# Kernel optimization log

Hardware: AMD Instinct MI355X
Metric: run time of the kernel (lower is better)

The kernel has to match this reference:

```python
import jax, jax.numpy as jnp
from jax import lax
import numpy as np

N = 10000      # nodes
T = 60         # lookback window
F = 16         # features per timestep
HL = 256       # lstm hidden dim
GH = 8         # gat heads
GC = 64        # gat out channels per head
GD = GH * GC   # 512 concat dim
FH = 512       # fusion hidden
E = 320000     # edges (before self loops)


def _lstm_layer(x, w_ih, w_hh, b_ih, b_hh):
    # x: [T, N, in] -> hidden sequence [T, N, HL]; torch gate order i,f,g,o
    n = x.shape[1]
    h0 = jnp.zeros((n, HL), x.dtype)
    def step(carry, xt):
        h, c = carry
        g = xt @ w_ih.T + h @ w_hh.T + b_ih + b_hh
        i, f, gg, o = jnp.split(g, 4, axis=-1)
        c = jax.nn.sigmoid(f) * c + jax.nn.sigmoid(i) * jnp.tanh(gg)
        h = jax.nn.sigmoid(o) * jnp.tanh(c)
        return (h, c), h
    _, hs = lax.scan(step, (h0, h0), x)
    return hs


def _gatv2(x, src, dst, ea, wl, bl, wr, br, we, att, bias):
    # GATv2Conv (concat=True, edge_dim=1, negative_slope=0.2); self loops already in src/dst/ea
    n = x.shape[0]
    xl = (x @ wl + bl).reshape(n, GH, GC)   # lin_l (source / x_j)
    xr = (x @ wr + br).reshape(n, GH, GC)   # lin_r (target / x_i)
    ee = (ea @ we).reshape(-1, GH, GC)      # lin_edge (bias=False)
    m = jax.nn.leaky_relu(xl[src] + xr[dst] + ee, 0.2)      # [E', GH, GC]
    logits = jnp.einsum('ehc,hc->eh', m, att)               # [E', GH]
    mx = jax.ops.segment_max(logits, dst, num_segments=n)
    ex = jnp.exp(logits - mx[dst])
    den = jax.ops.segment_sum(ex, dst, num_segments=n)
    alpha = ex / den[dst]                                   # softmax over in-edges per node
    out = jax.ops.segment_sum(xl[src] * alpha[..., None], dst, num_segments=n)
    return out.reshape(n, GD) + bias


def setup_inputs():
    key = jax.random.key(0)
    ks = jax.random.split(key, 20)
    f32 = jnp.float32
    def nrm(k, shp, fan):
        return jax.random.normal(k, shp, f32) * (1.0 / np.sqrt(fan))
    return {
        "x_seq": jax.random.normal(ks[0], (N, T, F), f32),
        "edge_index": jax.random.randint(ks[1], (2, E), 0, N, jnp.int32),
        "edge_attr": jax.random.uniform(ks[2], (E, 1), dtype=f32),
        "w_ih0": nrm(ks[3], (4 * HL, F), HL), "w_hh0": nrm(ks[4], (4 * HL, HL), HL),
        "b_ih0": jnp.zeros((4 * HL,), f32), "b_hh0": jnp.zeros((4 * HL,), f32),
        "w_ih1": nrm(ks[5], (4 * HL, HL), HL), "w_hh1": nrm(ks[6], (4 * HL, HL), HL),
        "b_ih1": jnp.zeros((4 * HL,), f32), "b_hh1": jnp.zeros((4 * HL,), f32),
        "g0_wl": nrm(ks[7], (HL, GD), HL), "g0_bl": jnp.zeros((GD,), f32),
        "g0_wr": nrm(ks[8], (HL, GD), HL), "g0_br": jnp.zeros((GD,), f32),
        "g0_we": nrm(ks[9], (1, GD), 1),
        "g0_att": nrm(ks[10], (GH, GC), GC), "g0_bias": jnp.zeros((GD,), f32),
        "g1_wl": nrm(ks[11], (GD, GD), GD), "g1_bl": jnp.zeros((GD,), f32),
        "g1_wr": nrm(ks[12], (GD, GD), GD), "g1_br": jnp.zeros((GD,), f32),
        "g1_we": nrm(ks[13], (1, GD), 1),
        "g1_att": nrm(ks[14], (GH, GC), GC), "g1_bias": jnp.zeros((GD,), f32),
        "fc1_w": nrm(ks[15], (HL + GD, FH), HL + GD), "fc1_b": jnp.zeros((FH,), f32),
        "fc2_w": nrm(ks[16], (FH, 1), FH), "fc2_b": jnp.zeros((1,), f32),
    }


def reference(x_seq, edge_index, edge_attr,
              w_ih0, w_hh0, b_ih0, b_hh0, w_ih1, w_hh1, b_ih1, b_hh1,
              g0_wl, g0_bl, g0_wr, g0_br, g0_we, g0_att, g0_bias,
              g1_wl, g1_bl, g1_wr, g1_br, g1_we, g1_att, g1_bias,
              fc1_w, fc1_b, fc2_w, fc2_b):
    # 2-layer LSTM encoder, take last timestep hidden (dropout off: eval mode)
    xt = jnp.transpose(x_seq, (1, 0, 2))            # [T, N, F]
    h1 = _lstm_layer(xt, w_ih0, w_hh0, b_ih0, b_hh0)
    h2 = _lstm_layer(h1, w_ih1, w_hh1, b_ih1, b_hh1)
    node = h2[-1]                                    # [N, HL]
    # add self loops; fill edge_attr for loops with mean (PyG default fill_value='mean')
    loop = jnp.arange(N, dtype=edge_index.dtype)
    src = jnp.concatenate([edge_index[0], loop])
    dst = jnp.concatenate([edge_index[1], loop])
    ea = jnp.concatenate([edge_attr, jnp.broadcast_to(edge_attr.mean(axis=0), (N, 1))], axis=0)
    g = jax.nn.elu(_gatv2(node, src, dst, ea, g0_wl, g0_bl, g0_wr, g0_br, g0_we, g0_att, g0_bias))
    g = jax.nn.elu(_gatv2(g, src, dst, ea, g1_wl, g1_bl, g1_wr, g1_br, g1_we, g1_att, g1_bias))
    fused = jnp.concatenate([node, g], axis=1)       # [N, HL+GD]
    h = jax.nn.relu(fused @ fc1_w + fc1_b)
    return h @ fc2_w + fc2_b                         # [N, 1]
```

## Files before the change

kernel.cpp:

```cpp
#include <hip/hip_runtime.h>

#define DEV __device__ __forceinline__

typedef _Float16 f16;
typedef _Float16 f16x8 __attribute__((ext_vector_type(8)));
typedef _Float16 f16x2 __attribute__((ext_vector_type(2)));
typedef float f32x4 __attribute__((ext_vector_type(4)));

DEV float sigmoidf_(float x) { return 1.0f / (1.0f + __expf(-x)); }
DEV float tanhf2_(float x)   { return 1.0f - 2.0f / (__expf(2.0f * x) + 1.0f); }

DEV void load_lds16(const void* g, void* l) {
    __builtin_amdgcn_global_load_lds(
        (const __attribute__((address_space(1))) char*)(const char*)g,
        (__attribute__((address_space(3))) char*)(unsigned int)(unsigned long long)(char*)l,
        16, 0, 0);
}

DEV int swz(int row, int ck) { return ck ^ (row & 3) ^ ((row >> 2) & 3); }

__global__ void prep_w0_kernel(const float* __restrict__ wih,
                               const float* __restrict__ whh,
                               f16* __restrict__ dst) {
    int idx = blockIdx.x * 256 + threadIdx.x;
    if (idx >= 1024 * 320) return;
    int rd = idx / 320, k = idx - rd * 320;
    int T = rd >> 7, p = rd & 127;
    int u = T * 32 + ((p >> 6) & 1) * 16 + (p & 15);
    int g = (p >> 4) & 3;
    int src = g * 256 + u;
    float v;
    if (k < 16)        v = wih[src * 16 + k];
    else if (k < 272)  v = whh[src * 256 + (k - 16)];
    else               v = 0.f;
    dst[idx] = (f16)v;
}

__global__ void prep_w1_kernel(const float* __restrict__ wih,
                               const float* __restrict__ whh,
                               f16* __restrict__ dst) {
    int idx = blockIdx.x * 256 + threadIdx.x;
    if (idx >= 1024 * 512) return;
    int rd = idx >> 9, k = idx & 511;
    int T = rd >> 7, p = rd & 127;
    int u = T * 32 + ((p >> 6) & 1) * 16 + (p & 15);
    int g = (p >> 4) & 3;
    int src = g * 256 + u;
    float v = (k < 256) ? wih[src * 256 + k] : whh[src * 256 + (k - 256)];
    dst[idx] = (f16)v;
}

__global__ void prep_bias4_kernel(const float* __restrict__ bi,
                                  const float* __restrict__ bh,
                                  float* __restrict__ dst) {
    int idx = blockIdx.x * 256 + threadIdx.x;
    if (idx >= 1024) return;
    int u = idx >> 2, g = idx & 3;
    dst[idx] = bi[g * 256 + u] + bh[g * 256 + u];
}

__global__ void prep_wt_kernel(const float* __restrict__ src, f16* __restrict__ dst,
                               int K, int N) {
    int idx = blockIdx.x * 256 + threadIdx.x;
    if (idx >= K * N) return;
    int n = idx / K, k = idx - n * K;
    dst[idx] = (f16)src[(size_t)k * N + n];
}

__global__ void prep_x0_kernel(const float* __restrict__ x_seq, f16* __restrict__ A0,
                               int Nn) {
    int idx = blockIdx.x * 256 + threadIdx.x;
    if (idx >= Nn * 16) return;
    int m = idx >> 4, f = idx & 15;
    A0[(size_t)m * 320 + f] = (f16)x_seq[(size_t)m * 960 + f];
}

DEV void tile_load_chunk(const f16* __restrict__ A, int lda,
                         const f16* __restrict__ Bt, int K,
                         int m0, int n0, int k0,
                         f16* __restrict__ sA, f16* __restrict__ sB,
                         int w, int arow, int achk)
{
#pragma unroll
    for (int c = 0; c < 2; ++c) {
        int R = c * 64 + w * 16;
        load_lds16(A + (size_t)(m0 + R + arow) * lda + k0 + achk, sA + R * 32);
        load_lds16(Bt + (size_t)(n0 + R + arow) * K + k0 + achk, sB + R * 32);
    }
}

DEV void tile_compute_chunk(const f16* __restrict__ sA, const f16* __restrict__ sB,
                            f32x4 (&acc)[4][4], int wr, int wc, int frow, int fsl)
{
    f16x8 af[4], bf[4];
#pragma unroll
    for (int i = 0; i < 4; ++i)
        af[i] = *(const f16x8*)&sA[(wr + i * 16 + frow) * 32 + fsl];
#pragma unroll
    for (int j = 0; j < 4; ++j)
        bf[j] = *(const f16x8*)&sB[(wc + j * 16 + frow) * 32 + fsl];
#pragma unroll
    for (int i = 0; i < 4; ++i)
#pragma unroll
        for (int j = 0; j < 4; ++j)
            acc[i][j] = __builtin_amdgcn_mfma_f32_16x16x32_f16(af[i], bf[j], acc[i][j], 0, 0, 0);
}

DEV void lstm_step_core(
    f16* __restrict__ sA, f16* __restrict__ sB,
    int bx, int by,
    const f16* __restrict__ A, int lda, int K,
    const f16* __restrict__ Wt,
    const float* __restrict__ bias4,
    float* __restrict__ c_state,
    f16* __restrict__ hA, int ldhA, int offhA,
    f16* __restrict__ hB, int ldhB, int offhB,
    const float* __restrict__ xsrc, int tnext,
    int M)
{
    const int tid = threadIdx.x;
    const int w = tid >> 6, lane = tid & 63;
    const int m0 = bx * 128, n0 = by * 128;
    const int arow = lane >> 2;
    const int achk = swz(arow, lane & 3) * 8;
    const int frow = lane & 15, l4 = lane >> 4;
    const int fsl = swz(frow, l4) * 8;
    const int wr = (w >> 1) * 64, wc = (w & 1) * 64;

    const int u = by * 32 + (w & 1) * 16 + (lane & 15);
    const int rbase = m0 + wr + (lane >> 4) * 4;
    float cold[4][4];
#pragma unroll
    for (int i = 0; i < 4; ++i)
#pragma unroll
        for (int r = 0; r < 4; ++r)
            cold[i][r] = c_state[(size_t)(rbase + i * 16 + r) * 256 + u];

    f32x4 acc[4][4] = {};
    const int nch = K >> 5;

    tile_load_chunk(A, lda, Wt, K, m0, n0, 0, sA, sB, w, arow, achk);
    for (int kc = 0; kc < nch; ++kc) {
        __syncthreads();
        const int cur = (kc & 1) * 4096;
        if (kc + 1 < nch) {
            const int nxt = ((kc + 1) & 1) * 4096;
            tile_load_chunk(A, lda, Wt, K, m0, n0, (kc + 1) * 32,
                            sA + nxt, sB + nxt, w, arow, achk);
        }
        tile_compute_chunk(sA + cur, sB + cur, acc, wr, wc, frow, fsl);
    }

    const float4 bb = *(const float4*)&bias4[u * 4];
#pragma unroll
    for (int i = 0; i < 4; ++i) {
#pragma unroll
        for (int r = 0; r < 4; ++r) {
            int m = rbase + i * 16 + r;
            if (m < M) {
                float gi = sigmoidf_(acc[i][0][r] + bb.x);
                float gf = sigmoidf_(acc[i][1][r] + bb.y);
                float gg = tanhf2_(acc[i][2][r] + bb.z);
                float go = sigmoidf_(acc[i][3][r] + bb.w);
                float cn = gf * cold[i][r] + gi * gg;
                c_state[(size_t)m * 256 + u] = cn;
                f16 h = (f16)(go * tanhf2_(cn));
                hA[(size_t)m * ldhA + offhA + u] = h;
                if (hB) hB[(size_t)m * ldhB + offhB + u] = h;
            }
        }
    }
    if (xsrc && by == 0) {
        int row = tid >> 1, fb = (tid & 1) * 8;
        int m = m0 + row;
        if (m < M) {
            const float* xp = xsrc + (size_t)m * 960 + tnext * 16 + fb;
            f16* dp = hB + (size_t)m * ldhB + fb;
#pragma unroll
            for (int q = 0; q < 8; ++q) dp[q] = (f16)xp[q];
        }
    }
}

__global__ __launch_bounds__(256) void lstm_mfma_kernel(
    const f16* __restrict__ A, int lda, int K,
    const f16* __restrict__ Wt, const float* __restrict__ bias4,
    float* __restrict__ c_state,
    f16* __restrict__ hA, int ldhA, int offhA,
    f16* __restrict__ hB, int ldhB, int offhB,
    const float* __restrict__ xsrc, int tnext, int M, int mtiles)
{
    __shared__ __align__(16) f16 sA[2 * 4096];
    __shared__ __align__(16) f16 sB[2 * 4096];
    const int l = blockIdx.x;
    const int xcd = l & 7, q = l >> 3;
    const int y = q & 7, xhi = q >> 3;
    const int x = xhi * 8 + xcd;
    if (x >= mtiles) return;
    lstm_step_core(sA, sB, x, y, A, lda, K, Wt, bias4, c_state,
                   hA, ldhA, offhA, hB, ldhB, offhB, xsrc, tnext, M);
}

__global__ __launch_bounds__(256) void lstm_dual_kernel(
    const f16* __restrict__ A1, const f16* __restrict__ W1t,
    const float* __restrict__ b41, float* __restrict__ c1,
    f16* __restrict__ h1A, int ldh1A, int offh1A,
    const f16* __restrict__ A0, const f16* __restrict__ W0t,
    const float* __restrict__ b40, float* __restrict__ c0,
    f16* __restrict__ h0A, int ldh0A, int offh0A,
    f16* __restrict__ h0B, int ldh0B, int offh0B,
    const float* __restrict__ xsrc, int tnext, int M, int mtiles)
{
    __shared__ __align__(16) f16 sA[2 * 4096];
    __shared__ __align__(16) f16 sB[2 * 4096];
    const int l = blockIdx.x;
    const int xcd = l & 7, q = l >> 3;
    const int yz = q & 15, xhi = q >> 4;
    const int x = xhi * 8 + xcd;
    if (x >= mtiles) return;
    const int y = yz & 7, z = yz >> 3;
    if (z == 0)
        lstm_step_core(sA, sB, x, y, A1, 512, 512, W1t, b41, c1,
                       h1A, ldh1A, offh1A, nullptr, 0, 0, nullptr, 0, M);
    else
        lstm_step_core(sA, sB, x, y, A0, 320, 320, W0t, b40, c0,
                       h0A, ldh0A, offh0A, h0B, ldh0B, offh0B, xsrc, tnext, M);
}

__global__ __launch_bounds__(256) void gemm16_kernel(
    const f16* __restrict__ A, int lda,
    const f16* __restrict__ Bt, int K,
    const float* __restrict__ bias,
    f16* __restrict__ C16, float* __restrict__ C32, int ldc,
    int act, int M)
{
    __shared__ __align__(16) f16 sA[2 * 4096];
    __shared__ __align__(16) f16 sB[2 * 4096];
    const int tid = threadIdx.x;
    const int w = tid >> 6, lane = tid & 63;
    const int m0 = blockIdx.x * 128, n0 = blockIdx.y * 128;
    const int arow = lane >> 2;
    const int achk = swz(arow, lane & 3) * 8;
    const int frow = lane & 15, l4 = lane >> 4;
    const int fsl = swz(frow, l4) * 8;
    const int wr = (w >> 1) * 64, wcn = (w & 1) * 64;

    f32x4 acc[4][4] = {};
    const int nch = K >> 5;

    tile_load_chunk(A, lda, Bt, K, m0, n0, 0, sA, sB, w, arow, achk);
    for (int kc = 0; kc < nch; ++kc) {
        __syncthreads();
        const int cur = (kc & 1) * 4096;
        if (kc + 1 < nch) {
            const int nxt = ((kc + 1) & 1) * 4096;
            tile_load_chunk(A, lda, Bt, K, m0, n0, (kc + 1) * 32,
                            sA + nxt, sB + nxt, w, arow, achk);
        }
        tile_compute_chunk(sA + cur, sB + cur, acc, wr, wcn, frow, fsl);
    }

    const int rbase = m0 + wr + (lane >> 4) * 4;
#pragma unroll
    for (int i = 0; i < 4; ++i) {
#pragma unroll
        for (int r = 0; r < 4; ++r) {
            int m = rbase + i * 16 + r;
            if (m >= M) continue;
#pragma unroll
            for (int j = 0; j < 4; ++j) {
                int n = n0 + wcn + j * 16 + (lane & 15);
                float v = acc[i][j][r] + bias[n];
                if (act == 1) v = fmaxf(v, 0.f);
                if (C16) C16[(size_t)m * ldc + n] = (f16)v;
                else     C32[(size_t)m * ldc + n] = v;
            }
        }
    }
}

__global__ __launch_bounds__(256) void gemm16_dual_kernel(
    const f16* __restrict__ A, int lda,
    const f16* __restrict__ Btl, const f16* __restrict__ Btr, int K,
    const float* __restrict__ biasl, const float* __restrict__ biasr,
    f16* __restrict__ Cl, f16* __restrict__ Cr, int ldc, int M)
{
    __shared__ __align__(16) f16 sA[2 * 4096];
    __shared__ __align__(16) f16 sB[2 * 4096];
    const int side = blockIdx.y >> 2;
    const f16* Bt = side ? Btr : Btl;
    const float* bias = side ? biasr : biasl;
    f16* C16 = side ? Cr : Cl;
    const int tid = threadIdx.x;
    const int w = tid >> 6, lane = tid & 63;
    const int m0 = blockIdx.x * 128, n0 = (blockIdx.y & 3) * 128;
    const int arow = lane >> 2;
    const int achk = swz(arow, lane & 3) * 8;
    const int frow = lane & 15, l4 = lane >> 4;
    const int fsl = swz(frow, l4) * 8;
    const int wr = (w >> 1) * 64, wcn = (w & 1) * 64;

    f32x4 acc[4][4] = {};
    const int nch = K >> 5;

    tile_load_chunk(A, lda, Bt, K, m0, n0, 0, sA, sB, w, arow, achk);
    for (int kc = 0; kc < nch; ++kc) {
        __syncthreads();
        const int cur = (kc & 1) * 4096;
        if (kc + 1 < nch) {
            const int nxt = ((kc + 1) & 1) * 4096;
            tile_load_chunk(A, lda, Bt, K, m0, n0, (kc + 1) * 32,
                            sA + nxt, sB + nxt, w, arow, achk);
        }
        tile_compute_chunk(sA + cur, sB + cur, acc, wr, wcn, frow, fsl);
    }

    const int rbase = m0 + wr + (lane >> 4) * 4;
#pragma unroll
    for (int i = 0; i < 4; ++i) {
#pragma unroll
        for (int r = 0; r < 4; ++r) {
            int m = rbase + i * 16 + r;
            if (m >= M) continue;
#pragma unroll
            for (int j = 0; j < 4; ++j) {
                int n = n0 + wcn + j * 16 + (lane & 15);
                float v = acc[i][j][r] + bias[n];
                C16[(size_t)m * ldc + n] = (f16)v;
            }
        }
    }
}

__global__ void mean_sum_kernel(const float* __restrict__ a, int n, float* __restrict__ out) {
    __shared__ float s[256];
    float loc = 0.f;
    for (int i = blockIdx.x * 256 + threadIdx.x; i < n; i += gridDim.x * 256) loc += a[i];
    s[threadIdx.x] = loc;
    __syncthreads();
    for (int off = 128; off; off >>= 1) {
        if (threadIdx.x < off) s[threadIdx.x] += s[threadIdx.x + off];
        __syncthreads();
    }
    if (threadIdx.x == 0) atomicAdd(out, s[0]);
}

__global__ void hist_kernel(const int* __restrict__ ei, int Ne, int Nn,
                            int* __restrict__ counts) {
    int e = blockIdx.x * 256 + threadIdx.x;
    if (e >= Ne + Nn) return;
    int d = (e < Ne) ? ei[Ne + e] : (e - Ne);
    atomicAdd(&counts[d], 1);
}

__global__ void scan_kernel(const int* __restrict__ counts, int* __restrict__ offsets, int n) {
    __shared__ int s[256];
    int tid = threadIdx.x;
    int chunk = (n + 255) / 256;
    int b = tid * chunk;
    int loc = 0;
    for (int j = 0; j < chunk; ++j) { int i = b + j; if (i < n) loc += counts[i]; }
    s[tid] = loc;
    __syncthreads();
    for (int off = 1; off < 256; off <<= 1) {
        int v = (tid >= off) ? s[tid - off] : 0;
        __syncthreads();
        s[tid] += v;
        __syncthreads();
    }
    int run = (tid == 0) ? 0 : s[tid - 1];
    for (int j = 0; j < chunk; ++j) {
        int i = b + j;
        if (i < n) { offsets[i] = run; run += counts[i]; }
    }
    if (tid == 255) offsets[n] = run;
}

__global__ void scatter_kernel(const int* __restrict__ ei, const float* __restrict__ ea,
                               const float* __restrict__ sump, float inv_ne, int Ne, int Nn,
                               int* __restrict__ cursor, int* __restrict__ src_sorted,
                               float* __restrict__ ea_sorted) {
    int e = blockIdx.x * 256 + threadIdx.x;
    if (e >= Ne + Nn) return;
    int s, d; float a;
    if (e < Ne) { s = ei[e]; d = ei[Ne + e]; a = ea[e]; }
    else        { s = e - Ne; d = s; a = sump[0] * inv_ne; }
    int pos = atomicAdd(&cursor[d], 1);
    src_sorted[pos] = s;
    ea_sorted[pos] = a;
}

__global__ __launch_bounds__(256) void gat_aggregate_kernel(
    const f16* __restrict__ xl, const f16* __restrict__ xr,
    const float* __restrict__ we, const float* __restrict__ att,
    const float* __restrict__ bias,
    const int* __restrict__ offsets, const int* __restrict__ src_sorted,
    const float* __restrict__ ea_sorted,
    float* __restrict__ logit_buf, f16* __restrict__ out, int ldo, int N)
{
    __shared__ float s_xr[512], s_we[512], s_att[512];
    __shared__ float s_wmax[32], s_mx[8], s_den[8], s_rden[8];
    __shared__ float s_alpha[256];
    __shared__ int s_src[32];
    const int i = blockIdx.x;
    const int tid = threadIdx.x;
    s_xr[tid]       = (float)xr[(size_t)i * 512 + tid];
    s_xr[tid + 256] = (float)xr[(size_t)i * 512 + tid + 256];
    s_we[tid] = we[tid]; s_we[tid + 256] = we[tid + 256];
    s_att[tid] = att[tid]; s_att[tid + 256] = att[tid + 256];
    if (tid < 8) s_den[tid] = 0.f;
    __syncthreads();

    const int beg = offsets[i], end = offsets[i + 1];
    const int w = tid >> 6, lane = tid & 63;

    float wm[4] = {-1e30f, -1e30f, -1e30f, -1e30f};
    for (int e = beg + w; e < end; e += 4) {
        int s = src_sorted[e];
        float a = ea_sorted[e];
        float part[4];
#pragma unroll
        for (int cc = 0; cc < 4; ++cc) {
            int col = cc * 128 + lane * 2;
            f16x2 xv = *(const f16x2*)&xl[(size_t)s * 512 + col];
            float v0 = (float)xv.x + s_xr[col]     + a * s_we[col];
            float v1 = (float)xv.y + s_xr[col + 1] + a * s_we[col + 1];
            v0 = (v0 > 0.f) ? v0 : 0.2f * v0;
            v1 = (v1 > 0.f) ? v1 : 0.2f * v1;
            part[cc] = v0 * s_att[col] + v1 * s_att[col + 1];
        }
#pragma unroll
        for (int off = 16; off; off >>= 1)
#pragma unroll
            for (int cc = 0; cc < 4; ++cc) part[cc] += __shfl_xor(part[cc], off);
        if ((lane & 31) == 0) {
            int hb = lane >> 5;
#pragma unroll
            for (int cc = 0; cc < 4; ++cc) {
                logit_buf[(size_t)e * 8 + 2 * cc + hb] = part[cc];
                wm[cc] = fmaxf(wm[cc], part[cc]);
            }
        }
    }
    if ((lane & 31) == 0) {
        int hb = lane >> 5;
#pragma unroll
        for (int cc = 0; cc < 4; ++cc) s_wmax[w * 8 + 2 * cc + hb] = wm[cc];
    }
    __syncthreads();
    if (tid < 8) {
        float m = fmaxf(fmaxf(s_wmax[tid], s_wmax[8 + tid]),
                        fmaxf(s_wmax[16 + tid], s_wmax[24 + tid]));
        s_mx[tid] = m;
    }
    __syncthreads();

    for (int e = beg + tid; e < end; e += 256) {
#pragma unroll
        for (int h = 0; h < 8; ++h) {
            float ex = __expf(logit_buf[(size_t)e * 8 + h] - s_mx[h]);
            logit_buf[(size_t)e * 8 + h] = ex;
            atomicAdd(&s_den[h], ex);
        }
    }
    __syncthreads();
    if (tid < 8) s_rden[tid] = 1.f / s_den[tid];
    __syncthreads();

    float acc0 = 0.f, acc1 = 0.f;
    const int c2 = tid * 2, hh = tid >> 5;
    for (int chunk = beg; chunk < end; chunk += 32) {
        int cnt = min(32, end - chunk);
        if (tid < cnt) s_src[tid] = src_sorted[chunk + tid];
        int eo = tid >> 3, hq = tid & 7;
        if (eo < cnt) s_alpha[tid] = logit_buf[(size_t)(chunk + eo) * 8 + hq] * s_rden[hq];
        __syncthreads();
        for (int j = 0; j < cnt; ++j) {
            int s = s_src[j];
            f16x2 xv = *(const f16x2*)&xl[(size_t)s * 512 + c2];
            float al = s_alpha[j * 8 + hh];
            acc0 += al * (float)xv.x;
            acc1 += al * (float)xv.y;
        }
        __syncthreads();
    }
    float v0 = acc0 + bias[c2];
    float v1 = acc1 + bias[c2 + 1];
    v0 = (v0 > 0.f) ? v0 : __expf(v0) - 1.f;
    v1 = (v1 > 0.f) ? v1 : __expf(v1) - 1.f;
    f16x2 ov; ov.x = (f16)v0; ov.y = (f16)v1;
    *(f16x2*)&out[(size_t)i * ldo + c2] = ov;
}

__global__ void fc2_kernel(const float* __restrict__ H, const float* __restrict__ w,
                           const float* __restrict__ b, float* __restrict__ out, int N) {
    int wv = threadIdx.x >> 6, lane = threadIdx.x & 63;
    int node = blockIdx.x * 4 + wv;
    if (node >= N) return;
    float s = 0.f;
#pragma unroll
    for (int j = 0; j < 8; ++j)
        s += H[(size_t)node * 512 + j * 64 + lane] * w[j * 64 + lane];
#pragma unroll
    for (int off = 32; off; off >>= 1) s += __shfl_xor(s, off, 64);
    if (lane == 0) out[node] = s + b[0];
}

extern "C" void kernel_launch(void* const* d_in, const int* in_sizes, int n_in,
                              void* d_out, int out_size, void* d_ws, size_t ws_size,
                              hipStream_t stream) {
    const float* x_seq     = (const float*)d_in[0];
    const int*   edge_index= (const int*)d_in[1];
    const float* edge_attr = (const float*)d_in[2];
    const float* w_ih0 = (const float*)d_in[3];
    const float* w_hh0 = (const float*)d_in[4];
    const float* b_ih0 = (const float*)d_in[5];
    const float* b_hh0 = (const float*)d_in[6];
    const float* w_ih1 = (const float*)d_in[7];
    const float* w_hh1 = (const float*)d_in[8];
    const float* b_ih1 = (const float*)d_in[9];
    const float* b_hh1 = (const float*)d_in[10];
    const float* g0_wl = (const float*)d_in[11];
    const float* g0_bl = (const float*)d_in[12];
    const float* g0_wr = (const float*)d_in[13];
    const float* g0_br = (const float*)d_in[14];
    const float* g0_we = (const float*)d_in[15];
    const float* g0_att= (const float*)d_in[16];
    const float* g0_bias=(const float*)d_in[17];
    const float* g1_wl = (const float*)d_in[18];
    const float* g1_bl = (const float*)d_in[19];
    const float* g1_wr = (const float*)d_in[20];
    const float* g1_br = (const float*)d_in[21];
    const float* g1_we = (const float*)d_in[22];
    const float* g1_att= (const float*)d_in[23];
    const float* g1_bias=(const float*)d_in[24];
    const float* fc1_w = (const float*)d_in[25];
    const float* fc1_b = (const float*)d_in[26];
    const float* fc2_w = (const float*)d_in[27];
    const float* fc2_b = (const float*)d_in[28];
    float* out = (float*)d_out;

    const int Nn = in_sizes[0] / (60 * 16);
    const int Ne = in_sizes[1] / 2;
    const int Etot = Ne + Nn;
    const int MT = (Nn + 127) / 128;
    const int Mpad = MT * 128;
    const int MTpad8 = ((MT + 7) / 8) * 8;

    size_t off = 0;
    auto alloc = [&](size_t bytes) -> void* {
        void* r = (char*)d_ws + off;
        off += (bytes + 255) & ~(size_t)255;
        return r;
    };
    f16* W0t   = (f16*)alloc((size_t)1024 * 320 * 2);
    f16* W1t   = (f16*)alloc((size_t)1024 * 512 * 2);
    float* b40 = (float*)alloc(1024 * 4);
    float* b41 = (float*)alloc(1024 * 4);
    f16* Wg0l  = (f16*)alloc((size_t)512 * 256 * 2);
    f16* Wg0r  = (f16*)alloc((size_t)512 * 256 * 2);
    f16* Wg1l  = (f16*)alloc((size_t)512 * 512 * 2);
    f16* Wg1r  = (f16*)alloc((size_t)512 * 512 * 2);
    f16* Wfc1  = (f16*)alloc((size_t)512 * 768 * 2);
    f16* A0b[2]; A0b[0] = (f16*)alloc((size_t)Mpad * 320 * 2);
                 A0b[1] = (f16*)alloc((size_t)Mpad * 320 * 2);
    f16* A1b[2]; A1b[0] = (f16*)alloc((size_t)Mpad * 512 * 2);
                 A1b[1] = (f16*)alloc((size_t)Mpad * 512 * 2);
    float* c0  = (float*)alloc((size_t)Mpad * 256 * 4);
    float* c1  = (float*)alloc((size_t)Mpad * 256 * 4);
    f16* fused = (f16*)alloc((size_t)Mpad * 768 * 2);
    f16* xlbuf = (f16*)alloc((size_t)Mpad * 512 * 2);
    f16* xrbuf = (f16*)alloc((size_t)Mpad * 512 * 2);
    f16* gbuf  = (f16*)alloc((size_t)Mpad * 512 * 2);
    float* hfc1= (float*)alloc((size_t)Mpad * 512 * 4);
    float* logit_buf = (float*)alloc((size_t)Etot * 8 * 4);
    int* counts  = (int*)alloc((size_t)Nn * 4);
    int* offsets = (int*)alloc((size_t)(Nn + 1) * 4);
    int* cursor  = (int*)alloc((size_t)Nn * 4);
    int* src_sorted = (int*)alloc((size_t)Etot * 4);
    float* ea_sorted = (float*)alloc((size_t)Etot * 4);
    float* meanp = (float*)alloc(256);

    prep_w0_kernel<<<dim3((1024 * 320 + 255) / 256), 256, 0, stream>>>(w_ih0, w_hh0, W0t);
    prep_w1_kernel<<<dim3((1024 * 512 + 255) / 256), 256, 0, stream>>>(w_ih1, w_hh1, W1t);
    prep_bias4_kernel<<<dim3(4), 256, 0, stream>>>(b_ih0, b_hh0, b40);
    prep_bias4_kernel<<<dim3(4), 256, 0, stream>>>(b_ih1, b_hh1, b41);
    prep_wt_kernel<<<dim3((256 * 512 + 255) / 256), 256, 0, stream>>>(g0_wl, Wg0l, 256, 512);
    prep_wt_kernel<<<dim3((256 * 512 + 255) / 256), 256, 0, stream>>>(g0_wr, Wg0r, 256, 512);
    prep_wt_kernel<<<dim3((512 * 512 + 255) / 256), 256, 0, stream>>>(g1_wl, Wg1l, 512, 512);
    prep_wt_kernel<<<dim3((512 * 512 + 255) / 256), 256, 0, stream>>>(g1_wr, Wg1r, 512, 512);
    prep_wt_kernel<<<dim3((768 * 512 + 255) / 256), 256, 0, stream>>>(fc1_w, Wfc1, 768, 512);
    hipMemsetAsync(A0b[0], 0, (size_t)Mpad * 320 * 2, stream);
    hipMemsetAsync(A0b[1], 0, (size_t)Mpad * 320 * 2, stream);
    hipMemsetAsync(A1b[0], 0, (size_t)Mpad * 512 * 2, stream);
    hipMemsetAsync(c0, 0, (size_t)Mpad * 256 * 4, stream);
    hipMemsetAsync(c1, 0, (size_t)Mpad * 256 * 4, stream);
    prep_x0_kernel<<<dim3((Nn * 16 + 255) / 256), 256, 0, stream>>>(x_seq, A0b[0], Nn);

    hipMemsetAsync(meanp, 0, 4, stream);
    hipMemsetAsync(counts, 0, (size_t)Nn * 4, stream);
    mean_sum_kernel<<<dim3(256), 256, 0, stream>>>(edge_attr, Ne, meanp);
    hist_kernel<<<dim3((Etot + 255) / 256), 256, 0, stream>>>(edge_index, Ne, Nn, counts);
    scan_kernel<<<dim3(1), 256, 0, stream>>>(counts, offsets, Nn);
    hipMemcpyAsync(cursor, offsets, (size_t)Nn * 4, hipMemcpyDeviceToDevice, stream);
    scatter_kernel<<<dim3((Etot + 255) / 256), 256, 0, stream>>>(
        edge_index, edge_attr, meanp, 1.0f / (float)Ne, Ne, Nn, cursor, src_sorted, ea_sorted);

    const int solo_grid = MTpad8 * 8;
    const int dual_grid = MTpad8 * 16;
    lstm_mfma_kernel<<<dim3(solo_grid), 256, 0, stream>>>(
        A0b[0], 320, 320, W0t, b40, c0,
        A1b[0], 512, 0,
        A0b[1], 320, 16,
        x_seq, 1, Nn, MT);
    for (int k = 0; k < 59; ++k) {
        lstm_dual_kernel<<<dim3(dual_grid), 256, 0, stream>>>(
            A1b[k & 1], W1t, b41, c1,
            A1b[(k + 1) & 1], 512, 256,
            A0b[(k + 1) & 1], W0t, b40, c0,
            A1b[(k + 1) & 1], 512, 0,
            A0b[k & 1], 320, 16,
            (k + 1 < 59) ? x_seq : nullptr, k + 2, Nn, MT);
    }
    lstm_mfma_kernel<<<dim3(solo_grid), 256, 0, stream>>>(
        A1b[1], 512, 512, W1t, b41, c1,
        fused, 768, 0,
        nullptr, 0, 0,
        nullptr, 0, Nn, MT);

    gemm16_dual_kernel<<<dim3(MT, 8), 256, 0, stream>>>(
        fused, 768, Wg0l, Wg0r, 256, g0_bl, g0_br, xlbuf, xrbuf, 512, Nn);
    gat_aggregate_kernel<<<dim3(Nn), 256, 0, stream>>>(
        xlbuf, xrbuf, g0_we, g0_att, g0_bias, offsets, src_sorted, ea_sorted,
        logit_buf, gbuf, 512, Nn);

    gemm16_dual_kernel<<<dim3(MT, 8), 256, 0, stream>>>(
        gbuf, 512, Wg1l, Wg1r, 512, g1_bl, g1_br, xlbuf, xrbuf, 512, Nn);
    gat_aggregate_kernel<<<dim3(Nn), 256, 0, stream>>>(
        xlbuf, xrbuf, g1_we, g1_att, g1_bias, offsets, src_sorted, ea_sorted,
        logit_buf, fused + 256, 768, Nn);

    gemm16_kernel<<<dim3(MT, 4), 256, 0, stream>>>(
        fused, 768, Wfc1, 768, fc1_b, nullptr, hfc1, 512, 1, Nn);
    fc2_kernel<<<dim3((Nn + 3) / 4), 256, 0, stream>>>(hfc1, fc2_w, fc2_b, out, Nn);
}
```

Measured before the change: 3.076 ms.

## Fuse GAT softmax into single-pass online aggregation and shrink layer-0 LSTM K padding

The three-pass GAT aggregation (logits to global buffer, exp/denominator, weighted sum) becomes one online-softmax pass. Each thread owns two channels, the per-head logit is reduced with 32-lane shuffles, and the next edge's source row is prefetched. This removes the logit buffer traffic, several block barriers and the shared-memory atomics, at the cost of serial per-edge exp rescaling. Separately, the layer-0 LSTM K dimension is padded to 288 instead of 320, which cuts MFMA work and loads per step provided the tile loop handles 288.

```diff
diff --git a/kernel.cpp b/kernel.cpp
--- a/kernel.cpp
+++ b/kernel.cpp
@@ -23,8 +23,8 @@
                                const float* __restrict__ whh,
                                f16* __restrict__ dst) {
     int idx = blockIdx.x * 256 + threadIdx.x;
-    if (idx >= 1024 * 320) return;
-    int rd = idx / 320, k = idx - rd * 320;
+    if (idx >= 1024 * 288) return;
+    int rd = idx / 288, k = idx - rd * 288;
     int T = rd >> 7, p = rd & 127;
     int u = T * 32 + ((p >> 6) & 1) * 16 + (p & 15);
     int g = (p >> 4) & 3;
@@ -72,7 +72,7 @@
     int idx = blockIdx.x * 256 + threadIdx.x;
     if (idx >= Nn * 16) return;
     int m = idx >> 4, f = idx & 15;
-    A0[(size_t)m * 320 + f] = (f16)x_seq[(size_t)m * 960 + f];
+    A0[(size_t)m * 288 + f] = (f16)x_seq[(size_t)m * 960 + f];
 }
 
 DEV void tile_load_chunk(const f16* __restrict__ A, int lda,
@@ -223,7 +223,7 @@
         lstm_step_core(sA, sB, x, y, A1, 512, 512, W1t, b41, c1,
                        h1A, ldh1A, offh1A, nullptr, 0, 0, nullptr, 0, M);
     else
-        lstm_step_core(sA, sB, x, y, A0, 320, 320, W0t, b40, c0,
+        lstm_step_core(sA, sB, x, y, A0, 288, 288, W0t, b40, c0,
                        h0A, ldh0A, offh0A, h0B, ldh0B, offh0B, xsrc, tnext, M);
 }
 
@@ -390,102 +390,61 @@
     ea_sorted[pos] = a;
 }
 
-__global__ __launch_bounds__(256) void gat_aggregate_kernel(
+__global__ __launch_bounds__(256) void gat_fused_kernel(
     const f16* __restrict__ xl, const f16* __restrict__ xr,
     const float* __restrict__ we, const float* __restrict__ att,
     const float* __restrict__ bias,
     const int* __restrict__ offsets, const int* __restrict__ src_sorted,
     const float* __restrict__ ea_sorted,
-    float* __restrict__ logit_buf, f16* __restrict__ out, int ldo, int N)
-{
-    __shared__ float s_xr[512], s_we[512], s_att[512];
-    __shared__ float s_wmax[32], s_mx[8], s_den[8], s_rden[8];
-    __shared__ float s_alpha[256];
-    __shared__ int s_src[32];
+    f16* __restrict__ out, int ldo, int N)
+{
     const int i = blockIdx.x;
     const int tid = threadIdx.x;
-    s_xr[tid]       = (float)xr[(size_t)i * 512 + tid];
-    s_xr[tid + 256] = (float)xr[(size_t)i * 512 + tid + 256];
-    s_we[tid] = we[tid]; s_we[tid + 256] = we[tid + 256];
-    s_att[tid] = att[tid]; s_att[tid + 256] = att[tid + 256];
-    if (tid < 8) s_den[tid] = 0.f;
-    __syncthreads();
+    const int c2 = tid * 2;
+
+    f16x2 xrv = *(const f16x2*)&xr[(size_t)i * 512 + c2];
+    const float xr0 = (float)xrv.x, xr1 = (float)xrv.y;
+    const float we0 = we[c2], we1 = we[c2 + 1];
+    const float at0 = att[c2], at1 = att[c2 + 1];
 
     const int beg = offsets[i], end = offsets[i + 1];
-    const int w = tid >> 6, lane = tid & 63;
-
-    float wm[4] = {-1e30f, -1e30f, -1e30f, -1e30f};
-    for (int e = beg + w; e < end; e += 4) {
-        int s = src_sorted[e];
-        float a = ea_sorted[e];
-        float part[4];
-#pragma unroll
-        for (int cc = 0; cc < 4; ++cc) {
-            int col = cc * 128 + lane * 2;
-            f16x2 xv = *(const f16x2*)&xl[(size_t)s * 512 + col];
-            float v0 = (float)xv.x + s_xr[col]     + a * s_we[col];
-            float v1 = (float)xv.y + s_xr[col + 1] + a * s_we[col + 1];
-            v0 = (v0 > 0.f) ? v0 : 0.2f * v0;
-            v1 = (v1 > 0.f) ? v1 : 0.2f * v1;
-            part[cc] = v0 * s_att[col] + v1 * s_att[col + 1];
-        }
-#pragma unroll
-        for (int off = 16; off; off >>= 1)
-#pragma unroll
-            for (int cc = 0; cc < 4; ++cc) part[cc] += __shfl_xor(part[cc], off);
-        if ((lane & 31) == 0) {
-            int hb = lane >> 5;
-#pragma unroll
-            for (int cc = 0; cc < 4; ++cc) {
-                logit_buf[(size_t)e * 8 + 2 * cc + hb] = part[cc];
-                wm[cc] = fmaxf(wm[cc], part[cc]);
-            }
-        }
-    }
-    if ((lane & 31) == 0) {
-        int hb = lane >> 5;
-#pragma unroll
-        for (int cc = 0; cc < 4; ++cc) s_wmax[w * 8 + 2 * cc + hb] = wm[cc];
-    }
-    __syncthreads();
-    if (tid < 8) {
-        float m = fmaxf(fmaxf(s_wmax[tid], s_wmax[8 + tid]),
-                        fmaxf(s_wmax[16 + tid], s_wmax[24 + tid]));
-        s_mx[tid] = m;
-    }
-    __syncthreads();
-
-    for (int e = beg + tid; e < end; e += 256) {
-#pragma unroll
-        for (int h = 0; h < 8; ++h) {
-            float ex = __expf(logit_buf[(size_t)e * 8 + h] - s_mx[h]);
-            logit_buf[(size_t)e * 8 + h] = ex;
-            atomicAdd(&s_den[h], ex);
-        }
-    }
-    __syncthreads();
-    if (tid < 8) s_rden[tid] = 1.f / s_den[tid];
-    __syncthreads();
-
-    float acc0 = 0.f, acc1 = 0.f;
-    const int c2 = tid * 2, hh = tid >> 5;
-    for (int chunk = beg; chunk < end; chunk += 32) {
-        int cnt = min(32, end - chunk);
-        if (tid < cnt) s_src[tid] = src_sorted[chunk + tid];
-        int eo = tid >> 3, hq = tid & 7;
-        if (eo < cnt) s_alpha[tid] = logit_buf[(size_t)(chunk + eo) * 8 + hq] * s_rden[hq];
-        __syncthreads();
-        for (int j = 0; j < cnt; ++j) {
-            int s = s_src[j];
-            f16x2 xv = *(const f16x2*)&xl[(size_t)s * 512 + c2];
-            float al = s_alpha[j * 8 + hh];
-            acc0 += al * (float)xv.x;
-            acc1 += al * (float)xv.y;
-        }
-        __syncthreads();
-    }
-    float v0 = acc0 + bias[c2];
-    float v1 = acc1 + bias[c2 + 1];
+
+    float m = -1e30f, den = 0.f, acc0 = 0.f, acc1 = 0.f;
+
+    float a = ea_sorted[beg];
+    f16x2 xv = *(const f16x2*)&xl[(size_t)src_sorted[beg] * 512 + c2];
+
+    for (int e = beg; e < end; ++e) {
+        float an = a; f16x2 xvn = xv;
+        if (e + 1 < end) {
+            int sn = src_sorted[e + 1];
+            an = ea_sorted[e + 1];
+            xvn = *(const f16x2*)&xl[(size_t)sn * 512 + c2];
+        }
+        float x0 = (float)xv.x, x1 = (float)xv.y;
+        float v0 = x0 + xr0 + a * we0;
+        float v1 = x1 + xr1 + a * we1;
+        v0 = (v0 > 0.f) ? v0 : 0.2f * v0;
+        v1 = (v1 > 0.f) ? v1 : 0.2f * v1;
+        float p = v0 * at0 + v1 * at1;
+        p += __shfl_xor(p, 1);
+        p += __shfl_xor(p, 2);
+        p += __shfl_xor(p, 4);
+        p += __shfl_xor(p, 8);
+        p += __shfl_xor(p, 16);
+        float mn = fmaxf(m, p);
+        float r  = __expf(m - mn);
+        float wg = __expf(p - mn);
+        acc0 = acc0 * r + wg * x0;
+        acc1 = acc1 * r + wg * x1;
+        den  = den * r + wg;
+        m = mn;
+        a = an; xv = xvn;
+    }
+
+    float rden = 1.f / den;
+    float v0 = acc0 * rden + bias[c2];
+    float v1 = acc1 * rden + bias[c2 + 1];
     v0 = (v0 > 0.f) ? v0 : __expf(v0) - 1.f;
     v1 = (v1 > 0.f) ? v1 : __expf(v1) - 1.f;
     f16x2 ov; ov.x = (f16)v0; ov.y = (f16)v1;
@@ -553,7 +512,7 @@
         off += (bytes + 255) & ~(size_t)255;
         return r;
     };
-    f16* W0t   = (f16*)alloc((size_t)1024 * 320 * 2);
+    f16* W0t   = (f16*)alloc((size_t)1024 * 288 * 2);
     f16* W1t   = (f16*)alloc((size_t)1024 * 512 * 2);
     float* b40 = (float*)alloc(1024 * 4);
     float* b41 = (float*)alloc(1024 * 4);
@@ -562,8 +521,8 @@
     f16* Wg1l  = (f16*)alloc((size_t)512 * 512 * 2);
     f16* Wg1r  = (f16*)alloc((size_t)512 * 512 * 2);
     f16* Wfc1  = (f16*)alloc((size_t)512 * 768 * 2);
-    f16* A0b[2]; A0b[0] = (f16*)alloc((size_t)Mpad * 320 * 2);
-                 A0b[1] = (f16*)alloc((size_t)Mpad * 320 * 2);
+    f16* A0b[2]; A0b[0] = (f16*)alloc((size_t)Mpad * 288 * 2);
+                 A0b[1] = (f16*)alloc((size_t)Mpad * 288 * 2);
     f16* A1b[2]; A1b[0] = (f16*)alloc((size_t)Mpad * 512 * 2);
                  A1b[1] = (f16*)alloc((size_t)Mpad * 512 * 2);
     float* c0  = (float*)alloc((size_t)Mpad * 256 * 4);
@@ -573,7 +532,6 @@
     f16* xrbuf = (f16*)alloc((size_t)Mpad * 512 * 2);
     f16* gbuf  = (f16*)alloc((size_t)Mpad * 512 * 2);
     float* hfc1= (float*)alloc((size_t)Mpad * 512 * 4);
-    float* logit_buf = (float*)alloc((size_t)Etot * 8 * 4);
     int* counts  = (int*)alloc((size_t)Nn * 4);
     int* offsets = (int*)alloc((size_t)(Nn + 1) * 4);
     int* cursor  = (int*)alloc((size_t)Nn * 4);
@@ -581,7 +539,7 @@
     float* ea_sorted = (float*)alloc((size_t)Etot * 4);
     float* meanp = (float*)alloc(256);
 
-    prep_w0_kernel<<<dim3((1024 * 320 + 255) / 256), 256, 0, stream>>>(w_ih0, w_hh0, W0t);
+    prep_w0_kernel<<<dim3((1024 * 288 + 255) / 256), 256, 0, stream>>>(w_ih0, w_hh0, W0t);
     prep_w1_kernel<<<dim3((1024 * 512 + 255) / 256), 256, 0, stream>>>(w_ih1, w_hh1, W1t);
     prep_bias4_kernel<<<dim3(4), 256, 0, stream>>>(b_ih0, b_hh0, b40);
     prep_bias4_kernel<<<dim3(4), 256, 0, stream>>>(b_ih1, b_hh1, b41);
@@ -590,8 +548,8 @@
     prep_wt_kernel<<<dim3((512 * 512 + 255) / 256), 256, 0, stream>>>(g1_wl, Wg1l, 512, 512);
     prep_wt_kernel<<<dim3((512 * 512 + 255) / 256), 256, 0, stream>>>(g1_wr, Wg1r, 512, 512);
     prep_wt_kernel<<<dim3((768 * 512 + 255) / 256), 256, 0, stream>>>(fc1_w, Wfc1, 768, 512);
-    hipMemsetAsync(A0b[0], 0, (size_t)Mpad * 320 * 2, stream);
-    hipMemsetAsync(A0b[1], 0, (size_t)Mpad * 320 * 2, stream);
+    hipMemsetAsync(A0b[0], 0, (size_t)Mpad * 288 * 2, stream);
+    hipMemsetAsync(A0b[1], 0, (size_t)Mpad * 288 * 2, stream);
     hipMemsetAsync(A1b[0], 0, (size_t)Mpad * 512 * 2, stream);
     hipMemsetAsync(c0, 0, (size_t)Mpad * 256 * 4, stream);
     hipMemsetAsync(c1, 0, (size_t)Mpad * 256 * 4, stream);
@@ -609,9 +567,9 @@
     const int solo_grid = MTpad8 * 8;
     const int dual_grid = MTpad8 * 16;
     lstm_mfma_kernel<<<dim3(solo_grid), 256, 0, stream>>>(
-        A0b[0], 320, 320, W0t, b40, c0,
+        A0b[0], 288, 288, W0t, b40, c0,
         A1b[0], 512, 0,
-        A0b[1], 320, 16,
+        A0b[1], 288, 16,
         x_seq, 1, Nn, MT);
     for (int k = 0; k < 59; ++k) {
         lstm_dual_kernel<<<dim3(dual_grid), 256, 0, stream>>>(
@@ -619,7 +577,7 @@
             A1b[(k + 1) & 1], 512, 256,
             A0b[(k + 1) & 1], W0t, b40, c0,
             A1b[(k + 1) & 1], 512, 0,
-            A0b[k & 1], 320, 16,
+            A0b[k & 1], 288, 16,
             (k + 1 < 59) ? x_seq : nullptr, k + 2, Nn, MT);
     }
     lstm_mfma_kernel<<<dim3(solo_grid), 256, 0, stream>>>(
@@ -630,15 +588,15 @@
 
     gemm16_dual_kernel<<<dim3(MT, 8), 256, 0, stream>>>(
         fused, 768, Wg0l, Wg0r, 256, g0_bl, g0_br, xlbuf, xrbuf, 512, Nn);
-    gat_aggregate_kernel<<<dim3(Nn), 256, 0, stream>>>(
+    gat_fused_kernel<<<dim3(Nn), 256, 0, stream>>>(
         xlbuf, xrbuf, g0_we, g0_att, g0_bias, offsets, src_sorted, ea_sorted,
-        logit_buf, gbuf, 512, Nn);
+        gbuf, 512, Nn);
 
     gemm16_dual_kernel<<<dim3(MT, 8), 256, 0, stream>>>(
         gbuf, 512, Wg1l, Wg1r, 512, g1_bl, g1_br, xlbuf, xrbuf, 512, Nn);
-    gat_aggregate_kernel<<<dim3(Nn), 256, 0, stream>>>(
+    gat_fused_kernel<<<dim3(Nn), 256, 0, stream>>>(
         xlbuf, xrbuf, g1_we, g1_att, g1_bias, offsets, src_sorted, ea_sorted,
-        logit_buf, fused + 256, 768, Nn);
+        fused + 256, 768, Nn);
 
     gemm16_kernel<<<dim3(MT, 4), 256, 0, stream>>>(
         fused, 768, Wfc1, 768, fc1_b, nullptr, hfc1, 512, 1, Nn);
```

Result: faster. 2.943 ms (-4.4%).
